# Optimization experiments

Hardware: AMD Instinct MI355X
Metric: run time of the kernel (lower is better)

The kernel has to match this reference:

```python
import jax, jax.numpy as jnp
import numpy as np
from jax import lax

B_SZ, D_SPEC, P, NC, MLP_D = 4096, 30, 9, 64, 64
L = P * P + 1  # 82 tokens (81 spiral + cls)


def _spiral_idx(patch=P):
    # Replicates Scan.forward's hardcoded assignments_map: center pixel, then
    # concentric rings (top row, right col, bottom row, left col), each of length 2r.
    cen = patch // 2
    rows, cols = [cen], [cen]
    for r in range(1, cen + 1):
        rows += [cen - r] * (2 * r); cols += list(range(cen - r + 1, cen + r + 1))
        rows += list(range(cen - r + 1, cen + r + 1)); cols += [cen + r] * (2 * r)
        rows += [cen + r] * (2 * r); cols += list(range(cen - r, cen + r))
        rows += list(range(cen - r, cen + r)); cols += [cen - r] * (2 * r)
    return np.asarray(rows), np.asarray(cols)

_ROWS, _COLS = _spiral_idx()


def _ln(x, g, b, eps=1e-5):
    m = x.mean(-1, keepdims=True)
    v = ((x - m) ** 2).mean(-1, keepdims=True)
    return (x - m) * lax.rsqrt(v + eps) * g + b


def _bn(x, g, b, m, v, nspatial, eps=1e-5):
    sh = (1, -1) + (1,) * nspatial
    return (x - m.reshape(sh)) * lax.rsqrt(v.reshape(sh) + eps) * g.reshape(sh) + b.reshape(sh)


def setup_inputs():
    key = jax.random.key(0)
    ks = iter(jax.random.split(key, 40))
    def rn(shape, s=0.1):
        return s * jax.random.normal(next(ks), shape, jnp.float32)
    return {
        "input_data": jax.random.normal(next(ks), (B_SZ, 1, D_SPEC, P, P), jnp.float32),
        "w3": rn((8, 1, 3, 3, 3)), "b3": rn((8,)),
        "g3": 1.0 + rn((8,)), "be3": rn((8,)), "m3": jnp.zeros((8,)), "v3": jnp.ones((8,)),
        "w2c": rn((NC, 8 * D_SPEC, 3, 3)), "b2c": rn((NC,)),
        "g2": 1.0 + rn((NC,)), "be2": rn((NC,)), "m2": jnp.zeros((NC,)), "v2": jnp.ones((NC,)),
        "pos_emb": rn((1, L, NC)), "cls_tok": rn((1, 1, NC)),
        "ln1_g": jnp.ones((NC,)), "ln1_b": jnp.zeros((NC,)),
        "Wb": rn((NC, NC)), "bb": rn((NC,)),
        "Wc": rn((NC, NC)), "bc": rn((NC,)),
        "Wd": rn((NC, NC)), "bd": rn((NC,)),
        "delta_p": rn((1, L, NC)), "A_p": rn((L, NC)),
        "Wst": rn((NC, NC)), "bst": rn((NC,)), "bias_st": rn((1, 1, NC)),
        "ln2_g": jnp.ones((NC,)), "ln2_b": jnp.zeros((NC,)),
        "Wm1": rn((NC, MLP_D)), "bm1": rn((MLP_D,)),
        "Wm2": rn((MLP_D, NC)), "bm2": rn((NC,)),
    }


def _forward(input_data, w3, b3, g3, be3, m3, v3, w2c, b2c, g2, be2, m2, v2,
             pos_emb, cls_tok, ln1_g, ln1_b, Wb, bb, Wc, bc, Wd, bd,
             delta_p, A_p, Wst, bst, bias_st, ln2_g, ln2_b, Wm1, bm1, Wm2, bm2):
    b = input_data.shape[0]
    # conv3d (SAME, k=3) + BN(eval) + ReLU
    h = lax.conv_general_dilated(input_data, w3, (1, 1, 1), [(1, 1)] * 3,
                                 dimension_numbers=("NCDHW", "OIDHW", "NCDHW"))
    h = jax.nn.relu(_bn(h + b3[None, :, None, None, None], g3, be3, m3, v3, 3))
    h = h.reshape(b, 8 * D_SPEC, P, P)  # 'b c h w y -> b (c h) w y'
    # conv2d (SAME, k=3) + BN(eval) + ReLU
    h = lax.conv_general_dilated(h, w2c, (1, 1), [(1, 1)] * 2,
                                 dimension_numbers=("NCHW", "OIHW", "NCHW"))
    h = jax.nn.relu(_bn(h + b2c[None, :, None, None], g2, be2, m2, v2, 2))
    # spiral scan gather: [B,C,H,W] -> [B,81,C]
    seq = jnp.transpose(h, (0, 2, 3, 1))[:, _ROWS, _COLS, :]
    tok = jnp.concatenate([jnp.broadcast_to(cls_tok, (b, 1, NC)), seq], axis=1) + pos_emb
    # (emb dropout = identity in eval)
    # --- Residual(LayerNormalize(S6_noC)) ---
    xn = _ln(tok, ln1_g, ln1_b)
    z = jax.nn.sigmoid(xn)
    B0 = xn @ Wb + bb
    C_ = xn @ Wc + bc
    sq = jnp.mean(xn, axis=1, keepdims=True)              # SToken squeeze [B,1,D]
    sq = jax.nn.sigmoid(jax.nn.relu(sq @ Wst + bst))
    T_ = (sq + bias_st) * xn                              # [B,L,D]
    delta = jax.nn.sigmoid(xn @ Wd + bd + delta_p)
    A_ = delta * A_p[None]                                # [B,L,D]
    Bx = delta * B0 * xn                                  # B_ * x fused
    def step(s, inp):
        a, bx, c, t = inp
        s = a * s + bx
        return s, c * s + t
    ins = (jnp.moveaxis(A_, 1, 0), jnp.moveaxis(Bx, 1, 0),
           jnp.moveaxis(C_, 1, 0), jnp.moveaxis(T_, 1, 0))  # [L,B,D]
    _, out = lax.scan(step, jnp.zeros((b, NC), xn.dtype), ins)
    tok = tok + jnp.moveaxis(out, 0, 1) * z               # residual
    # AdaptiveAvgPool1d(1) over seq + squeeze -> [B, D]
    pooled = tok.mean(axis=1)
    # --- Residual(LayerNormalize(MLP_Block)) (dropout = identity) ---
    yn = _ln(pooled, ln2_g, ln2_b)
    mlp = jax.nn.gelu(yn @ Wm1 + bm1, approximate=False) @ Wm2 + bm2
    return pooled + mlp


def reference(input_data, w3, b3, g3, be3, m3, v3, w2c, b2c, g2, be2, m2, v2,
              pos_emb, cls_tok, ln1_g, ln1_b, Wb, bb, Wc, bc, Wd, bd,
              delta_p, A_p, Wst, bst, bias_st, ln2_g, ln2_b, Wm1, bm1, Wm2, bm2):
    return _forward(input_data, w3, b3, g3, be3, m3, v3, w2c, b2c, g2, be2, m2, v2,
                    pos_emb, cls_tok, ln1_g, ln1_b, Wb, bb, Wc, bc, Wd, bd,
                    delta_p, A_p, Wst, bst, bias_st, ln2_g, ln2_b, Wm1, bm1, Wm2, bm2)
```

## Files before the change

kernel.cpp:

```cpp
#include <hip/hip_runtime.h>

typedef unsigned short u16;
typedef __attribute__((ext_vector_type(8))) short bf16x8;
typedef __attribute__((ext_vector_type(4))) float f32x4;
typedef __attribute__((ext_vector_type(4))) int i32x4;

#define DEV __device__ __forceinline__

DEV u16 f2bf(float f){
  unsigned u = __float_as_uint(f);
  u += 0x7fffu + ((u >> 16) & 1u);
  return (u16)(u >> 16);
}
DEV float bf2f(u16 h){ return __uint_as_float(((unsigned)h) << 16); }

DEV int spiral_t(int pix){
  int px = pix / 9, py = pix % 9;
  int dr = px - 4, dc = py - 4;
  int ar = dr < 0 ? -dr : dr, ac = dc < 0 ? -dc : dc;
  int r = ar > ac ? ar : ac;
  if (r == 0) return 0;
  int start = 1 + 4*r*(r-1);
  if (dr == -r && dc >= -r+1) return start + dc + r - 1;
  if (dc == r)  return start + 2*r + dr + r - 1;
  if (dr == r)  return start + 4*r + dc + r;
  return start + 6*r + dr + r;
}

__global__ __launch_bounds__(256) void k_wt(const float* __restrict__ w2c,
                                            const float* __restrict__ g2,
                                            const float* __restrict__ v2,
                                            u16* __restrict__ Wt2){
  int idx = blockIdx.x*256 + threadIdx.x;
  if (idx >= 72*64*32) return;
  int kk = idx & 31;
  int o  = (idx >> 5) & 63;
  int tile = idx >> 11;
  int dxy = tile >> 3;
  int chunk = tile & 7;
  int ch = chunk*32 + kk;
  float v = 0.f;
  if (ch < 240){
    float s2 = g2[o] * rsqrtf(v2[o] + 1e-5f);
    v = w2c[(o*240 + ch)*9 + dxy] * s2;
  }
  Wt2[idx] = f2bf(v);
}

__global__ __launch_bounds__(256) void k_conv3d(const float* __restrict__ x,
    const float* __restrict__ w3, const float* __restrict__ b3,
    const float* __restrict__ g3, const float* __restrict__ be3,
    const float* __restrict__ m3, const float* __restrict__ v3,
    u16* __restrict__ h1){
  __shared__ float tile[3872];
  __shared__ float wle[216];
  __shared__ float sc[8], sh[8];
  int b = blockIdx.x, tid = threadIdx.x;
  for (int i = tid; i < 3872; i += 256) tile[i] = 0.f;
  if (tid < 216) wle[tid] = w3[tid];
  if (tid < 8){
    float s = g3[tid]*rsqrtf(v3[tid]+1e-5f);
    sc[tid] = s;
    sh[tid] = (b3[tid]-m3[tid])*s + be3[tid];
  }
  __syncthreads();
  const float* xin = x + b*2430;
  for (int i = tid; i < 2430; i += 256){
    int dd = i / 81, rem = i % 81;
    int px = rem / 9, py = rem % 9;
    tile[(dd+1)*121 + (px+1)*11 + (py+1)] = xin[i];
  }
  __syncthreads();
  u16* hb = h1 + (size_t)b*19440;
  for (int p = tid; p < 2430; p += 256){
    int pix = p / 30, dd = p % 30;
    int px = pix / 9, py = pix % 9;
    const float* tp = tile + dd*121 + px*11 + py;
    float v[27];
    #pragma unroll
    for (int kd=0;kd<3;kd++)
      #pragma unroll
      for (int kx=0;kx<3;kx++)
        #pragma unroll
        for (int ky=0;ky<3;ky++)
          v[(kd*3+kx)*3+ky] = tp[kd*121 + kx*11 + ky];
    u16* hp = hb + pix*240 + dd;
    #pragma unroll
    for (int co=0;co<8;co++){
      float acc = 0.f;
      const float* wp = wle + co*27;
      #pragma unroll
      for (int q=0;q<27;q++) acc = fmaf(v[q], wp[q], acc);
      hp[co*30] = f2bf(fmaxf(acc*sc[co] + sh[co], 0.f));
    }
  }
}

__global__ __launch_bounds__(256, 2) void k_conv2d(const u16* __restrict__ h1,
    const u16* __restrict__ Wt2,
    const float* __restrict__ b2c, const float* __restrict__ g2,
    const float* __restrict__ be2, const float* __restrict__ m2,
    const float* __restrict__ v2,
    const float* __restrict__ pos_emb, const float* __restrict__ cls_tok,
    const float* __restrict__ ln1_g, const float* __restrict__ ln1_b,
    const float* __restrict__ Wst, const float* __restrict__ bst,
    const float* __restrict__ bias_st,
    u16* __restrict__ xn, float* __restrict__ tsum, float* __restrict__ sqs){
  __shared__ __align__(16) char smem[80848];
  const int ZROW = 80352;
  int tid = threadIdx.x;
  int wv = tid >> 6, ln = tid & 63;
  int lq = ln >> 4, lr = ln & 15;
  int img0 = blockIdx.x*2;
  size_t grow0 = (size_t)img0*81;

  int bln = lr*32 + lq*8;

#define LOADB(TAP, C, B)                                                        \
    { const u16* Bt_ = Wt2 + (TAP)*16384 + bln;                                 \
      _Pragma("unroll")                                                         \
      for (int kk=0;kk<2;kk++)                                                  \
        _Pragma("unroll")                                                       \
        for (int j=0;j<4;j++)                                                   \
          B[kk][j] = *(const bf16x8*)(Bt_ + ((C)*2+kk)*2048 + j*512); }

  bf16x8 bB0[2][4], bB1[2][4], bB2[2][4];
  LOADB(0, 0, bB0);
  LOADB(0, 1, bB1);
  LOADB(0, 2, bB2);

  for (int r = tid; r < 162; r += 256)
    *(i32x4*)(smem + r*496 + 480) = (i32x4){0,0,0,0};
  if (tid < 31) *(i32x4*)(smem + ZROW + tid*16) = (i32x4){0,0,0,0};
  {
    const u16* src = h1 + grow0*240;
    for (int idx = tid; idx < 162*30; idx += 256){
      int r = idx / 30, c = idx % 30;
      *(i32x4*)(smem + r*496 + c*16) = *(const i32x4*)(src + idx*8);
    }
  }
  __syncthreads();

  f32x4 acc[3][4];
  #pragma unroll
  for (int i=0;i<3;i++)
    #pragma unroll
    for (int j=0;j<4;j++) acc[i][j] = (f32x4){0.f,0.f,0.f,0.f};

#define CALCADDR(TAP, A0, A1, A13)                                              \
  { int dx = (TAP)/3 - 1, dy = (TAP)%3 - 1;                                     \
    _Pragma("unroll")                                                           \
    for (int rt=0;rt<3;rt++){                                                   \
      int row = (wv*3+rt)*16 + lr;                                              \
      int pix = row % 81;                                                       \
      int px = pix/9, py = pix%9;                                               \
      int px2 = px + dx, py2 = py + dy;                                         \
      bool valid = (row < 162) && ((unsigned)px2 < 9u) && ((unsigned)py2 < 9u); \
      int nrow = (row - pix) + px2*9 + py2;                                     \
      int base = valid ? nrow*496 : ZROW;                                       \
      A0[rt]  = base + lq*16;                                                   \
      A1[rt]  = base + 64 + lq*16;                                              \
      A13[rt] = (lq == 3) ? ZROW : (A1[rt] + 384);                              \
    } }

#define LOADA(C, SA0, SA1, SA13, A0, A1)                                        \
    { _Pragma("unroll")                                                         \
      for (int rt=0;rt<3;rt++){                                                 \
        A0[rt] = *(const bf16x8*)(smem + SA0[rt] + (C)*128);                    \
        A1[rt] = *(const bf16x8*)(smem + ((C)==3 ? SA13[rt]                     \
                                                 : SA1[rt] + (C)*128)); } }

#define DOMFMA(B, A0, A1)                                                       \
    { __builtin_amdgcn_s_setprio(1);                                            \
      _Pragma("unroll")                                                         \
      for (int rt=0;rt<3;rt++)                                                  \
        _Pragma("unroll")                                                       \
        for (int j=0;j<4;j++)                                                   \
          acc[rt][j] = __builtin_amdgcn_mfma_f32_16x16x32_bf16(A0[rt], B[0][j], acc[rt][j], 0, 0, 0); \
      _Pragma("unroll")                                                         \
      for (int rt=0;rt<3;rt++)                                                  \
        _Pragma("unroll")                                                       \
        for (int j=0;j<4;j++)                                                   \
          acc[rt][j] = __builtin_amdgcn_mfma_f32_16x16x32_bf16(A1[rt], B[1][j], acc[rt][j], 0, 0, 0); \
      __builtin_amdgcn_s_setprio(0); }

#define TAPBODY(TAPV, BA, BB, BC)                                               \
  { int ntap_ = (TAPV) < 8 ? (TAPV)+1 : 8;                                      \
    DOMFMA(BA, aAX0, aAX1);                                                     \
    LOADB((TAPV), 3, BA); LOADA(2, aC0, aC1, aC13, aAX0, aAX1);                 \
    DOMFMA(BB, aAY0, aAY1);                                                     \
    LOADB(ntap_, 0, BB); CALCADDR(ntap_, aN0, aN1, aN13);                       \
    LOADA(3, aC0, aC1, aC13, aAY0, aAY1);                                       \
    DOMFMA(BC, aAX0, aAX1);                                                     \
    LOADB(ntap_, 1, BC); LOADA(0, aN0, aN1, aN13, aAX0, aAX1);                  \
    DOMFMA(BA, aAY0, aAY1);                                                     \
    LOADB(ntap_, 2, BA); LOADA(1, aN0, aN1, aN13, aAY0, aAY1);                  \
    _Pragma("unroll")                                                           \
    for (int rt=0;rt<3;rt++){ aC0[rt]=aN0[rt]; aC1[rt]=aN1[rt]; aC13[rt]=aN13[rt]; } }

  int aC0[3], aC1[3], aC13[3];
  int aN0[3], aN1[3], aN13[3];
  bf16x8 aAX0[3], aAX1[3], aAY0[3], aAY1[3];

  CALCADDR(0, aC0, aC1, aC13);
  LOADA(0, aC0, aC1, aC13, aAX0, aAX1);
  LOADA(1, aC0, aC1, aC13, aAY0, aAY1);

  for (int t3 = 0; t3 < 9; t3 += 3){
    TAPBODY(t3+0, bB0, bB1, bB2);
    TAPBODY(t3+1, bB1, bB2, bB0);
    TAPBODY(t3+2, bB2, bB0, bB1);
  }
#undef CALCADDR
#undef LOADB
#undef LOADA
#undef DOMFMA
#undef TAPBODY

  __syncthreads();

  float t2c[4], lg[4], lb[4];
  #pragma unroll
  for (int j=0;j<4;j++){
    int col = j*16 + lr;
    float s2 = g2[col]*rsqrtf(v2[col]+1e-5f);
    t2c[j] = (b2c[col]-m2[col])*s2 + be2[col];
    lg[j] = ln1_g[col]; lb[j] = ln1_b[col];
  }

  float st0[4]={0,0,0,0}, st1[4]={0,0,0,0};
  float sx0[4]={0,0,0,0}, sx1[4]={0,0,0,0};

  #pragma unroll
  for (int rt=0;rt<3;rt++){
    #pragma unroll
    for (int e=0;e<4;e++){
      int row = (wv*3+rt)*16 + lq*4 + e;
      if (row < 162){
        int im = (row >= 81);
        int pix = row - im*81;
        int tsp = spiral_t(pix);
        const float* pe = pos_emb + (1+tsp)*64;
        float y[4], m1 = 0.f, m2v = 0.f;
        #pragma unroll
        for (int j=0;j<4;j++){
          y[j] = fmaxf(acc[rt][j][e] + t2c[j], 0.f) + pe[j*16+lr];
          m1 += y[j]; m2v = fmaf(y[j], y[j], m2v);
        }
        #pragma unroll
        for (int off=1; off<16; off<<=1){
          m1  += __shfl_xor(m1,  off, 64);
          m2v += __shfl_xor(m2v, off, 64);
        }
        float mean = m1*(1.f/64.f);
        float var  = m2v*(1.f/64.f) - mean*mean;
        float rs = rsqrtf(var + 1e-5f);
        u16* dst = xn + ((size_t)(img0+im)*82 + 1 + tsp)*64;
        #pragma unroll
        for (int j=0;j<4;j++){
          float xnv = (y[j]-mean)*rs*lg[j] + lb[j];
          dst[j*16+lr] = f2bf(xnv);
          if (im == 0){ st0[j] += y[j]; sx0[j] += xnv; }
          else        { st1[j] += y[j]; sx1[j] += xnv; }
        }
      }
    }
  }

  #pragma unroll
  for (int j=0;j<4;j++){
    st0[j] += __shfl_xor(st0[j],16,64); st0[j] += __shfl_xor(st0[j],32,64);
    st1[j] += __shfl_xor(st1[j],16,64); st1[j] += __shfl_xor(st1[j],32,64);
    sx0[j] += __shfl_xor(sx0[j],16,64); sx0[j] += __shfl_xor(sx0[j],32,64);
    sx1[j] += __shfl_xor(sx1[j],16,64); sx1[j] += __shfl_xor(sx1[j],32,64);
  }
  float* partT = (float*)smem;
  float* partX = (float*)(smem + 2048);
  float* xsumL = (float*)(smem + 4096);
  if (lq == 0){
    #pragma unroll
    for (int j=0;j<4;j++){
      partT[wv*128 +       j*16+lr] = st0[j];
      partT[wv*128 + 64  + j*16+lr] = st1[j];
      partX[wv*128 +       j*16+lr] = sx0[j];
      partX[wv*128 + 64  + j*16+lr] = sx1[j];
    }
  }
  __syncthreads();
  if (tid < 128){
    int im = tid >> 6, d = tid & 63;
    float tt = partT[im*64+d] + partT[128+im*64+d] + partT[256+im*64+d] + partT[384+im*64+d];
    float xx = partX[im*64+d] + partX[128+im*64+d] + partX[256+im*64+d] + partX[384+im*64+d];
    float clsv = cls_tok[d] + pos_emb[d];
    float c1 = clsv, c2 = clsv*clsv;
    #pragma unroll
    for (int off=1; off<64; off<<=1){ c1 += __shfl_xor(c1, off, 64); c2 += __shfl_xor(c2, off, 64); }
    float cm = c1*(1.f/64.f), cv = c2*(1.f/64.f) - cm*cm;
    float cxn = (clsv - cm)*rsqrtf(cv + 1e-5f)*ln1_g[d] + ln1_b[d];
    xn[((size_t)(img0+im)*82)*64 + d] = f2bf(cxn);
    tsum[(size_t)(img0+im)*64 + d] = tt + clsv;
    xsumL[im*64 + d] = (xx + cxn) * (1.f/82.f);
  }
  __syncthreads();
  {
    int im = tid >> 7, d2 = tid & 127;
    int d = d2 >> 1, half = d2 & 1;
    float a = 0.f;
    int k0 = half*32;
    #pragma unroll
    for (int k=0;k<32;k++) a = fmaf(xsumL[im*64 + k0+k], Wst[(k0+k)*64+d], a);
    a += __shfl_xor(a, 1, 64);
    if (half == 0){
      a += bst[d];
      a = fmaxf(a, 0.f);
      a = 1.f/(1.f + __expf(-a));
      sqs[(size_t)(img0+im)*64 + d] = a + bias_st[d];
    }
  }
}

__global__ __launch_bounds__(256, 1) void k_bcd(const u16* __restrict__ xn,
    const float* __restrict__ Wb, const float* __restrict__ Wc, const float* __restrict__ Wd,
    const float* __restrict__ bbv, const float* __restrict__ bcv,
    const float* __restrict__ bdv,
    const float* __restrict__ delta_p, const float* __restrict__ A_p,
    u16* __restrict__ Ax, u16* __restrict__ Bxx, u16* __restrict__ Cx){
  __shared__ char At[16384];
  int tid = threadIdx.x;
  int wv = tid >> 6, ln = tid & 63;
  int lq = ln >> 4, lr = ln & 15;
  size_t r0 = (size_t)blockIdx.x * 128;

  {
    int row = tid >> 1, hh = tid & 1;
    const char* src = (const char*)xn + (r0 + row)*128 + hh*64;
    #pragma unroll
    for (int c=0;c<4;c++){
      i32x4 v = *(const i32x4*)(src + c*16);
      *(i32x4*)(At + row*128 + ((hh*64 + c*16) ^ ((row&7)<<4))) = v;
    }
  }

  bf16x8 bfr[2][12];
  #pragma unroll
  for (int kk=0;kk<2;kk++)
    #pragma unroll
    for (int j=0;j<12;j++){
      int c = j*16 + lr;
      const float* W = (c < 64) ? Wb : ((c < 128) ? Wc : Wd);
      int cc = c & 63;
      int k0 = kk*32 + lq*8;
      bf16x8 f;
      #pragma unroll
      for (int e=0;e<8;e++) f[e] = (short)f2bf(W[(k0+e)*64 + cc]);
      bfr[kk][j] = f;
    }
  __syncthreads();

  f32x4 acc[2][12];
  #pragma unroll
  for (int i=0;i<2;i++)
    #pragma unroll
    for (int j=0;j<12;j++) acc[i][j] = (f32x4){0.f,0.f,0.f,0.f};

  #pragma unroll
  for (int kk=0;kk<2;kk++){
    bf16x8 afr[2];
    #pragma unroll
    for (int i=0;i<2;i++){
      int row = wv*32 + i*16 + lr;
      afr[i] = *(const bf16x8*)(At + row*128 + ((kk*64 + lq*16) ^ ((row&7)<<4)));
    }
    #pragma unroll
    for (int i=0;i<2;i++)
      #pragma unroll
      for (int j=0;j<12;j++)
        acc[i][j] = __builtin_amdgcn_mfma_f32_16x16x32_bf16(afr[i], bfr[kk][j], acc[i][j], 0, 0, 0);
  }

  #pragma unroll
  for (int i=0;i<2;i++){
    #pragma unroll
    for (int e=0;e<4;e++){
      int row = wv*32 + i*16 + lq*4 + e;
      unsigned rr = (unsigned)(r0 + row);
      unsigned t = rr % 82u;
      #pragma unroll
      for (int j=0;j<4;j++){
        int d = j*16 + lr;
        float B0 = acc[i][j][e]   + bbv[d];
        float Cv = acc[i][j+4][e] + bcv[d];
        float Dr = acc[i][j+8][e] + bdv[d] + delta_p[t*64+d];
        float D  = 1.f/(1.f + __expf(-Dr));
        int byte = j*32 + lr*2;
        float xv = bf2f(*(const u16*)(At + row*128 + (byte ^ ((row&7)<<4))));
        size_t o = (size_t)rr*64 + d;
        Ax[o]  = f2bf(D * A_p[t*64+d]);
        Bxx[o] = f2bf(D * B0 * xv);
        Cx[o]  = f2bf(Cv);
      }
    }
  }
}

__global__ __launch_bounds__(256) void k_scan(const u16* __restrict__ xn,
    const u16* __restrict__ Ax, const u16* __restrict__ Bxx, const u16* __restrict__ Cx,
    const float* __restrict__ tsum, const float* __restrict__ sqs,
    const float* __restrict__ ln2_g, const float* __restrict__ ln2_b,
    const float* __restrict__ Wm1, const float* __restrict__ bm1,
    const float* __restrict__ Wm2, const float* __restrict__ bm2,
    float* __restrict__ out){
  int tid = threadIdx.x, wv = tid >> 6, d = tid & 63;
  int b = blockIdx.x*4 + wv;
  float sq = sqs[b*64 + d];
  float s = 0.f, racc = 0.f;
  size_t base = (size_t)b*82*64 + d;
  #pragma unroll 2
  for (int t = 0; t < 82; t++){
    float a  = bf2f(Ax[base]);
    float bx = bf2f(Bxx[base]);
    float c  = bf2f(Cx[base]);
    float xv = bf2f(xn[base]);
    s = fmaf(a, s, bx);
    float o = fmaf(c, s, sq*xv);
    float z = 1.f/(1.f + __expf(-xv));
    racc = fmaf(o, z, racc);
    base += 64;
  }
  float pooled = (tsum[b*64 + d] + racc) * (1.f/82.f);
  float s1 = pooled, s2v = pooled*pooled;
  #pragma unroll
  for (int off=32; off>0; off>>=1){ s1 += __shfl_xor(s1, off, 64); s2v += __shfl_xor(s2v, off, 64); }
  float mean = s1*(1.f/64.f), var = s2v*(1.f/64.f) - mean*mean;
  float yn = (pooled - mean)*rsqrtf(var + 1e-5f)*ln2_g[d] + ln2_b[d];
  float a1 = bm1[d];
  for (int k=0;k<64;k++) a1 = fmaf(__shfl(yn, k, 64), Wm1[k*64+d], a1);
  float hg = 0.5f*a1*(1.f + erff(a1*0.70710678118654752f));
  float a2 = bm2[d];
  for (int k=0;k<64;k++) a2 = fmaf(__shfl(hg, k, 64), Wm2[k*64+d], a2);
  out[b*64 + d] = pooled + a2;
}

extern "C" void kernel_launch(void* const* d_in, const int* in_sizes, int n_in,
                              void* d_out, int out_size, void* d_ws, size_t ws_size,
                              hipStream_t stream){
  const float* x       = (const float*)d_in[0];
  const float* w3      = (const float*)d_in[1];
  const float* b3      = (const float*)d_in[2];
  const float* g3      = (const float*)d_in[3];
  const float* be3     = (const float*)d_in[4];
  const float* m3      = (const float*)d_in[5];
  const float* v3      = (const float*)d_in[6];
  const float* w2c     = (const float*)d_in[7];
  const float* b2c     = (const float*)d_in[8];
  const float* g2      = (const float*)d_in[9];
  const float* be2     = (const float*)d_in[10];
  const float* m2      = (const float*)d_in[11];
  const float* v2      = (const float*)d_in[12];
  const float* pos_emb = (const float*)d_in[13];
  const float* cls_tok = (const float*)d_in[14];
  const float* ln1_g   = (const float*)d_in[15];
  const float* ln1_b   = (const float*)d_in[16];
  const float* Wb      = (const float*)d_in[17];
  const float* bbv     = (const float*)d_in[18];
  const float* Wc      = (const float*)d_in[19];
  const float* bc      = (const float*)d_in[20];
  const float* Wd      = (const float*)d_in[21];
  const float* bd      = (const float*)d_in[22];
  const float* delta_p = (const float*)d_in[23];
  const float* A_p     = (const float*)d_in[24];
  const float* Wst     = (const float*)d_in[25];
  const float* bst     = (const float*)d_in[26];
  const float* bias_st = (const float*)d_in[27];
  const float* ln2_g   = (const float*)d_in[28];
  const float* ln2_b   = (const float*)d_in[29];
  const float* Wm1     = (const float*)d_in[30];
  const float* bm1     = (const float*)d_in[31];
  const float* Wm2     = (const float*)d_in[32];
  const float* bm2     = (const float*)d_in[33];

  char* ws = (char*)d_ws;
  u16*   h1   = (u16*)ws;
  u16*   Wt2  = (u16*)(ws + 159252480);
  u16*   xnb  = (u16*)(ws + 159571968);
  float* tsum = (float*)(ws + 202563584);
  float* sqs  = (float*)(ws + 203612160);
  u16*   Ax   = (u16*)ws;
  u16*   Cx   = (u16*)(ws + 42991616);
  u16*   Bxx  = (u16*)(ws + 85983232);

  k_wt    <<<576,  256, 0, stream>>>(w2c, g2, v2, Wt2);
  k_conv3d<<<4096, 256, 0, stream>>>(x, w3, b3, g3, be3, m3, v3, h1);
  k_conv2d<<<2048, 256, 0, stream>>>(h1, Wt2, b2c, g2, be2, m2, v2,
                                     pos_emb, cls_tok, ln1_g, ln1_b,
                                     Wst, bst, bias_st, xnb, tsum, sqs);
  k_bcd   <<<2624, 256, 0, stream>>>(xnb, Wb, Wc, Wd, bbv, bc, bd, delta_p, A_p,
                                     Ax, Bxx, Cx);
  k_scan  <<<1024, 256, 0, stream>>>(xnb, Ax, Bxx, Cx, tsum, sqs,
                                     ln2_g, ln2_b, Wm1, bm1, Wm2, bm2, (float*)d_out);
}
```

Measured before the change: 407.0 us.

## Fuse B/C/D projection GEMM with selective scan and MLP head per image

Merges the k_bcd projection kernel and the k_scan recurrence kernel into one kernel that runs one block per image. The Ax/Bxx/Cx intermediates stay in shared memory instead of round-tripping through global memory. This removes roughly three 43MB bf16 write-plus-read passes and one launch. In exchange, only one wave of four runs the serial 82-step scan and the MLP, the B/C/D weights are re-converted to bf16 in every block, and the 96-row tile pads the 82 tokens, which wastes some MFMA work.

```diff
diff --git a/kernel.cpp b/kernel.cpp
--- a/kernel.cpp
+++ b/kernel.cpp
@@ -292,10 +292,10 @@
     float tt = partT[im*64+d] + partT[128+im*64+d] + partT[256+im*64+d] + partT[384+im*64+d];
     float xx = partX[im*64+d] + partX[128+im*64+d] + partX[256+im*64+d] + partX[384+im*64+d];
     float clsv = cls_tok[d] + pos_emb[d];
-    float c1 = clsv, c2 = clsv*clsv;
-    #pragma unroll
-    for (int off=1; off<64; off<<=1){ c1 += __shfl_xor(c1, off, 64); c2 += __shfl_xor(c2, off, 64); }
-    float cm = c1*(1.f/64.f), cv = c2*(1.f/64.f) - cm*cm;
+    float c1v = clsv, c2v = clsv*clsv;
+    #pragma unroll
+    for (int off=1; off<64; off<<=1){ c1v += __shfl_xor(c1v, off, 64); c2v += __shfl_xor(c2v, off, 64); }
+    float cm = c1v*(1.f/64.f), cv = c2v*(1.f/64.f) - cm*cm;
     float cxn = (clsv - cm)*rsqrtf(cv + 1e-5f)*ln1_g[d] + ln1_b[d];
     xn[((size_t)(img0+im)*82)*64 + d] = f2bf(cxn);
     tsum[(size_t)(img0+im)*64 + d] = tt + clsv;
@@ -319,126 +319,121 @@
   }
 }
 
-__global__ __launch_bounds__(256, 1) void k_bcd(const u16* __restrict__ xn,
+__global__ __launch_bounds__(256, 2) void k_fuse(const u16* __restrict__ xn,
+    const float* __restrict__ tsum, const float* __restrict__ sqs,
     const float* __restrict__ Wb, const float* __restrict__ Wc, const float* __restrict__ Wd,
-    const float* __restrict__ bbv, const float* __restrict__ bcv,
-    const float* __restrict__ bdv,
+    const float* __restrict__ bbv, const float* __restrict__ bcv, const float* __restrict__ bdv,
     const float* __restrict__ delta_p, const float* __restrict__ A_p,
-    u16* __restrict__ Ax, u16* __restrict__ Bxx, u16* __restrict__ Cx){
-  __shared__ char At[16384];
-  int tid = threadIdx.x;
-  int wv = tid >> 6, ln = tid & 63;
-  int lq = ln >> 4, lr = ln & 15;
-  size_t r0 = (size_t)blockIdx.x * 128;
-
-  {
-    int row = tid >> 1, hh = tid & 1;
-    const char* src = (const char*)xn + (r0 + row)*128 + hh*64;
-    #pragma unroll
-    for (int c=0;c<4;c++){
-      i32x4 v = *(const i32x4*)(src + c*16);
-      *(i32x4*)(At + row*128 + ((hh*64 + c*16) ^ ((row&7)<<4))) = v;
-    }
-  }
-
-  bf16x8 bfr[2][12];
-  #pragma unroll
-  for (int kk=0;kk<2;kk++)
-    #pragma unroll
-    for (int j=0;j<12;j++){
-      int c = j*16 + lr;
-      const float* W = (c < 64) ? Wb : ((c < 128) ? Wc : Wd);
-      int cc = c & 63;
-      int k0 = kk*32 + lq*8;
-      bf16x8 f;
-      #pragma unroll
-      for (int e=0;e<8;e++) f[e] = (short)f2bf(W[(k0+e)*64 + cc]);
-      bfr[kk][j] = f;
-    }
-  __syncthreads();
-
-  f32x4 acc[2][12];
-  #pragma unroll
-  for (int i=0;i<2;i++)
-    #pragma unroll
-    for (int j=0;j<12;j++) acc[i][j] = (f32x4){0.f,0.f,0.f,0.f};
-
-  #pragma unroll
-  for (int kk=0;kk<2;kk++){
-    bf16x8 afr[2];
-    #pragma unroll
-    for (int i=0;i<2;i++){
-      int row = wv*32 + i*16 + lr;
-      afr[i] = *(const bf16x8*)(At + row*128 + ((kk*64 + lq*16) ^ ((row&7)<<4)));
-    }
-    #pragma unroll
-    for (int i=0;i<2;i++)
-      #pragma unroll
-      for (int j=0;j<12;j++)
-        acc[i][j] = __builtin_amdgcn_mfma_f32_16x16x32_bf16(afr[i], bfr[kk][j], acc[i][j], 0, 0, 0);
-  }
-
-  #pragma unroll
-  for (int i=0;i<2;i++){
-    #pragma unroll
-    for (int e=0;e<4;e++){
-      int row = wv*32 + i*16 + lq*4 + e;
-      unsigned rr = (unsigned)(r0 + row);
-      unsigned t = rr % 82u;
-      #pragma unroll
-      for (int j=0;j<4;j++){
-        int d = j*16 + lr;
-        float B0 = acc[i][j][e]   + bbv[d];
-        float Cv = acc[i][j+4][e] + bcv[d];
-        float Dr = acc[i][j+8][e] + bdv[d] + delta_p[t*64+d];
-        float D  = 1.f/(1.f + __expf(-Dr));
-        int byte = j*32 + lr*2;
-        float xv = bf2f(*(const u16*)(At + row*128 + (byte ^ ((row&7)<<4))));
-        size_t o = (size_t)rr*64 + d;
-        Ax[o]  = f2bf(D * A_p[t*64+d]);
-        Bxx[o] = f2bf(D * B0 * xv);
-        Cx[o]  = f2bf(Cv);
-      }
-    }
-  }
-}
-
-__global__ __launch_bounds__(256) void k_scan(const u16* __restrict__ xn,
-    const u16* __restrict__ Ax, const u16* __restrict__ Bxx, const u16* __restrict__ Cx,
-    const float* __restrict__ tsum, const float* __restrict__ sqs,
     const float* __restrict__ ln2_g, const float* __restrict__ ln2_b,
     const float* __restrict__ Wm1, const float* __restrict__ bm1,
     const float* __restrict__ Wm2, const float* __restrict__ bm2,
     float* __restrict__ out){
-  int tid = threadIdx.x, wv = tid >> 6, d = tid & 63;
-  int b = blockIdx.x*4 + wv;
-  float sq = sqs[b*64 + d];
-  float s = 0.f, racc = 0.f;
-  size_t base = (size_t)b*82*64 + d;
-  #pragma unroll 2
-  for (int t = 0; t < 82; t++){
-    float a  = bf2f(Ax[base]);
-    float bx = bf2f(Bxx[base]);
-    float c  = bf2f(Cx[base]);
-    float xv = bf2f(xn[base]);
-    s = fmaf(a, s, bx);
-    float o = fmaf(c, s, sq*xv);
-    float z = 1.f/(1.f + __expf(-xv));
-    racc = fmaf(o, z, racc);
-    base += 64;
-  }
-  float pooled = (tsum[b*64 + d] + racc) * (1.f/82.f);
-  float s1 = pooled, s2v = pooled*pooled;
-  #pragma unroll
-  for (int off=32; off>0; off>>=1){ s1 += __shfl_xor(s1, off, 64); s2v += __shfl_xor(s2v, off, 64); }
-  float mean = s1*(1.f/64.f), var = s2v*(1.f/64.f) - mean*mean;
-  float yn = (pooled - mean)*rsqrtf(var + 1e-5f)*ln2_g[d] + ln2_b[d];
-  float a1 = bm1[d];
-  for (int k=0;k<64;k++) a1 = fmaf(__shfl(yn, k, 64), Wm1[k*64+d], a1);
-  float hg = 0.5f*a1*(1.f + erff(a1*0.70710678118654752f));
-  float a2 = bm2[d];
-  for (int k=0;k<64;k++) a2 = fmaf(__shfl(hg, k, 64), Wm2[k*64+d], a2);
-  out[b*64 + d] = pooled + a2;
+  __shared__ __align__(16) char xnL[96*128];
+  __shared__ u16 AxL[96][66], BxL[96][66], CxL[96][66];
+  int tid = threadIdx.x;
+  int wv = tid >> 6, ln = tid & 63;
+  int lq = ln >> 4, lr = ln & 15;
+  int b = blockIdx.x;
+
+  bf16x8 bfr[3][2];
+  {
+    int cc = wv*16 + lr;
+    const float* Ws[3] = {Wb, Wc, Wd};
+    #pragma unroll
+    for (int w=0;w<3;w++)
+      #pragma unroll
+      for (int kk=0;kk<2;kk++){
+        int k0 = kk*32 + lq*8;
+        bf16x8 f;
+        #pragma unroll
+        for (int e=0;e<8;e++) f[e] = (short)f2bf(Ws[w][(k0+e)*64 + cc]);
+        bfr[w][kk] = f;
+      }
+  }
+
+  {
+    const u16* src = xn + (size_t)b*82*64;
+    for (int idx = tid; idx < 656; idx += 256){
+      int r = idx >> 3, c = idx & 7;
+      *(i32x4*)(xnL + r*128 + ((c*16) ^ ((r&7)<<4))) = *(const i32x4*)(src + idx*8);
+    }
+    for (int idx = tid; idx < 112; idx += 256){
+      int r = 82 + (idx >> 3), c = idx & 7;
+      *(i32x4*)(xnL + r*128 + ((c*16) ^ ((r&7)<<4))) = (i32x4){0,0,0,0};
+    }
+  }
+  __syncthreads();
+
+  f32x4 acc[6][3];
+  #pragma unroll
+  for (int i=0;i<6;i++)
+    #pragma unroll
+    for (int w=0;w<3;w++) acc[i][w] = (f32x4){0.f,0.f,0.f,0.f};
+
+  #pragma unroll
+  for (int rt=0;rt<6;rt++){
+    int row = rt*16 + lr;
+    bf16x8 afr[2];
+    #pragma unroll
+    for (int kk=0;kk<2;kk++)
+      afr[kk] = *(const bf16x8*)(xnL + row*128 + ((kk*64 + lq*16) ^ ((row&7)<<4)));
+    #pragma unroll
+    for (int kk=0;kk<2;kk++)
+      #pragma unroll
+      for (int w=0;w<3;w++)
+        acc[rt][w] = __builtin_amdgcn_mfma_f32_16x16x32_bf16(afr[kk], bfr[w][kk], acc[rt][w], 0, 0, 0);
+  }
+
+  {
+    int d = wv*16 + lr;
+    float bB = bbv[d], bC = bcv[d], bD = bdv[d];
+    #pragma unroll
+    for (int rt=0;rt<6;rt++){
+      #pragma unroll
+      for (int e=0;e<4;e++){
+        int t = rt*16 + lq*4 + e;
+        if (t < 82){
+          float B0 = acc[rt][0][e] + bB;
+          float Cv = acc[rt][1][e] + bC;
+          float Dr = acc[rt][2][e] + bD + delta_p[t*64+d];
+          float D  = 1.f/(1.f + __expf(-Dr));
+          float xv = bf2f(*(const u16*)(xnL + t*128 + ((d*2) ^ ((t&7)<<4))));
+          AxL[t][d] = f2bf(D * A_p[t*64+d]);
+          BxL[t][d] = f2bf(D * B0 * xv);
+          CxL[t][d] = f2bf(Cv);
+        }
+      }
+    }
+  }
+  __syncthreads();
+
+  if (wv == 0){
+    int d = ln;
+    float sq = sqs[(size_t)b*64 + d];
+    float s = 0.f, racc = 0.f;
+    for (int t = 0; t < 82; t++){
+      float a  = bf2f(AxL[t][d]);
+      float bx = bf2f(BxL[t][d]);
+      float c  = bf2f(CxL[t][d]);
+      float xv = bf2f(*(const u16*)(xnL + t*128 + ((d*2) ^ ((t&7)<<4))));
+      s = fmaf(a, s, bx);
+      float o = fmaf(c, s, sq*xv);
+      float z = 1.f/(1.f + __expf(-xv));
+      racc = fmaf(o, z, racc);
+    }
+    float pooled = (tsum[(size_t)b*64 + d] + racc) * (1.f/82.f);
+    float s1 = pooled, s2v = pooled*pooled;
+    #pragma unroll
+    for (int off=32; off>0; off>>=1){ s1 += __shfl_xor(s1, off, 64); s2v += __shfl_xor(s2v, off, 64); }
+    float mean = s1*(1.f/64.f), var = s2v*(1.f/64.f) - mean*mean;
+    float yn = (pooled - mean)*rsqrtf(var + 1e-5f)*ln2_g[d] + ln2_b[d];
+    float a1 = bm1[d];
+    for (int k=0;k<64;k++) a1 = fmaf(__shfl(yn, k, 64), Wm1[k*64+d], a1);
+    float hg = 0.5f*a1*(1.f + erff(a1*0.70710678118654752f));
+    float a2 = bm2[d];
+    for (int k=0;k<64;k++) a2 = fmaf(__shfl(hg, k, 64), Wm2[k*64+d], a2);
+    out[(size_t)b*64 + d] = pooled + a2;
+  }
 }
 
 extern "C" void kernel_launch(void* const* d_in, const int* in_sizes, int n_in,
@@ -485,17 +480,13 @@
   u16*   xnb  = (u16*)(ws + 159571968);
   float* tsum = (float*)(ws + 202563584);
   float* sqs  = (float*)(ws + 203612160);
-  u16*   Ax   = (u16*)ws;
-  u16*   Cx   = (u16*)(ws + 42991616);
-  u16*   Bxx  = (u16*)(ws + 85983232);
 
   k_wt    <<<576,  256, 0, stream>>>(w2c, g2, v2, Wt2);
   k_conv3d<<<4096, 256, 0, stream>>>(x, w3, b3, g3, be3, m3, v3, h1);
   k_conv2d<<<2048, 256, 0, stream>>>(h1, Wt2, b2c, g2, be2, m2, v2,
                                      pos_emb, cls_tok, ln1_g, ln1_b,
                                      Wst, bst, bias_st, xnb, tsum, sqs);
-  k_bcd   <<<2624, 256, 0, stream>>>(xnb, Wb, Wc, Wd, bbv, bc, bd, delta_p, A_p,
-                                     Ax, Bxx, Cx);
-  k_scan  <<<1024, 256, 0, stream>>>(xnb, Ax, Bxx, Cx, tsum, sqs,
-                                     ln2_g, ln2_b, Wm1, bm1, Wm2, bm2, (float*)d_out);
-}
+  k_fuse  <<<4096, 256, 0, stream>>>(xnb, tsum, sqs, Wb, Wc, Wd, bbv, bc, bd,
+                                     delta_p, A_p, ln2_g, ln2_b,
+                                     Wm1, bm1, Wm2, bm2, (float*)d_out);
+}
```

Result: faster. 383.4 us (-5.8%).
